# Kernel tuning notes

Measured on AMD Instinct MI355X. Metric: run time of the kernel, lower is better.

Reference implementation:

```python
import jax, jax.numpy as jnp
import numpy as np

DIM = 768
HEADS = 12
HD = DIM // HEADS
B, NX, NY = 8, 1024, 1024
GRID = 32
FREQ = 100.0
MLP_HID = 4 * DIM
EPS = 1e-5


def _grid_pos(batch, n, grid):
    g = int(np.sqrt(n))
    yy, xx = jnp.meshgrid(jnp.arange(g, dtype=jnp.int32), jnp.arange(g, dtype=jnp.int32), indexing='ij')
    pos = jnp.stack([yy.reshape(-1), xx.reshape(-1)], axis=-1)  # [N,2]
    return jnp.broadcast_to(pos[None], (batch, n, 2))


def setup_inputs() -> dict:
    key = jax.random.key(0)
    ks = jax.random.split(key, 16)
    s = 0.02
    inp = {
        'x': jax.random.normal(ks[0], (B, NX, DIM), jnp.float32),
        'y': jax.random.normal(ks[1], (B, NY, DIM), jnp.float32),
        'xpos': _grid_pos(B, NX, GRID),
        'ypos': _grid_pos(B, NY, GRID),
        # norms (gamma, beta)
        'norm1_g': jnp.ones((DIM,), jnp.float32), 'norm1_b': jnp.zeros((DIM,), jnp.float32),
        'norm2_g': jnp.ones((DIM,), jnp.float32), 'norm2_b': jnp.zeros((DIM,), jnp.float32),
        'norm3_g': jnp.ones((DIM,), jnp.float32), 'norm3_b': jnp.zeros((DIM,), jnp.float32),
        'normy_g': jnp.ones((DIM,), jnp.float32), 'normy_b': jnp.zeros((DIM,), jnp.float32),
        # self-attn: fused qkv (no bias, qkv_bias=False), out proj (with bias)
        'qkv_w': jax.random.normal(ks[2], (DIM, 3 * DIM), jnp.float32) * s,
        'attn_proj_w': jax.random.normal(ks[3], (DIM, DIM), jnp.float32) * s,
        'attn_proj_b': jnp.zeros((DIM,), jnp.float32),
        # cross-attn: separate q/k/v (no bias), out proj (with bias)
        'projq_w': jax.random.normal(ks[4], (DIM, DIM), jnp.float32) * s,
        'projk_w': jax.random.normal(ks[5], (DIM, DIM), jnp.float32) * s,
        'projv_w': jax.random.normal(ks[6], (DIM, DIM), jnp.float32) * s,
        'cross_proj_w': jax.random.normal(ks[7], (DIM, DIM), jnp.float32) * s,
        'cross_proj_b': jnp.zeros((DIM,), jnp.float32),
        # MLP
        'fc1_w': jax.random.normal(ks[8], (DIM, MLP_HID), jnp.float32) * s,
        'fc1_b': jnp.zeros((MLP_HID,), jnp.float32),
        'fc2_w': jax.random.normal(ks[9], (MLP_HID, DIM), jnp.float32) * s,
        'fc2_b': jnp.zeros((DIM,), jnp.float32),
    }
    return inp


def layernorm(x, g, b):
    m = jnp.mean(x, axis=-1, keepdims=True)
    v = jnp.mean(jnp.square(x - m), axis=-1, keepdims=True)
    return (x - m) * jax.lax.rsqrt(v + EPS) * g + b


def rope1d(tok, pos):
    # tok: [B,H,N,D], pos: [B,N] int
    D = tok.shape[-1]
    inv = 1.0 / (FREQ ** (jnp.arange(0, D, 2, dtype=jnp.float32) / D))  # [D/2]
    f = pos[:, None, :, None].astype(jnp.float32) * inv  # [B,1,N,D/2]
    emb = jnp.concatenate([f, f], axis=-1)  # [B,1,N,D]
    cos, sin = jnp.cos(emb), jnp.sin(emb)
    t1, t2 = jnp.split(tok, 2, axis=-1)
    rot = jnp.concatenate([-t2, t1], axis=-1)
    return tok * cos + rot * sin


def rope2d(tok, pos):
    # first half of head dim rotated by y-coord, second half by x-coord
    ty, tx = jnp.split(tok, 2, axis=-1)
    return jnp.concatenate([rope1d(ty, pos[..., 0]), rope1d(tx, pos[..., 1])], axis=-1)


def sdpa(q, k, v):
    scale = q.shape[-1] ** -0.5
    a = jax.nn.softmax(jnp.einsum('bhqd,bhkd->bhqk', q, k) * scale, axis=-1)
    return jnp.einsum('bhqk,bhkd->bhqd', a, v)


def split_heads(t):  # [B,N,C] -> [B,H,N,HD]
    Bv, N, C = t.shape
    return t.reshape(Bv, N, HEADS, HD).transpose(0, 2, 1, 3)


def merge_heads(t):  # [B,H,N,HD] -> [B,N,C]
    Bv, H, N, D = t.shape
    return t.transpose(0, 2, 1, 3).reshape(Bv, N, H * D)


def reference(x, y, xpos, ypos,
              norm1_g, norm1_b, norm2_g, norm2_b, norm3_g, norm3_b, normy_g, normy_b,
              qkv_w, attn_proj_w, attn_proj_b,
              projq_w, projk_w, projv_w, cross_proj_w, cross_proj_b,
              fc1_w, fc1_b, fc2_w, fc2_b):
    # --- self attention ---
    h = layernorm(x, norm1_g, norm1_b)
    qkv = h @ qkv_w  # [B,N,3C]
    q, k, v = (split_heads(t) for t in jnp.split(qkv, 3, axis=-1))
    q = rope2d(q, xpos)
    k = rope2d(k, xpos)
    x = x + merge_heads(sdpa(q, k, v)) @ attn_proj_w + attn_proj_b

    # --- cross attention ---
    y_ = layernorm(y, normy_g, normy_b)
    hq = layernorm(x, norm2_g, norm2_b)
    q = rope2d(split_heads(hq @ projq_w), xpos)
    k = rope2d(split_heads(y_ @ projk_w), ypos)
    v = split_heads(y_ @ projv_w)
    x = x + merge_heads(sdpa(q, k, v)) @ cross_proj_w + cross_proj_b

    # --- MLP ---
    h = layernorm(x, norm3_g, norm3_b)
    x = x + jax.nn.gelu(h @ fc1_w + fc1_b, approximate=False) @ fc2_w + fc2_b
    return (x, y)
```

## Files before the change

### kernel.cpp

```cpp
#include <hip/hip_runtime.h>
#include <hip/hip_bf16.h>
#include <math.h>

#define DIM 768
#define HEADS 12
#define HD 64
#define BB 8
#define NN 1024
#define EPSV 1e-5f

typedef unsigned int uint32;
typedef unsigned short ushort_t;
using short8 = __attribute__((ext_vector_type(8))) short;
using f32x4 = __attribute__((ext_vector_type(4))) float;

static __device__ inline ushort_t f2b(float v) {
    uint32 u = __float_as_uint(v);
    return (ushort_t)((u + 0x7FFFu + ((u >> 16) & 1u)) >> 16);
}
static __device__ inline float b2f(ushort_t v) {
    return __uint_as_float((uint32)v << 16);
}

static __device__ inline float gelu_fast(float v) {
    float v2 = v * v;
    float t1 = fmaf(0.07135481283f, v2, 1.5957691216f);
    float e = __expf(-v * t1);
    return v * __frcp_rn(1.0f + e);
}

static __device__ __forceinline__ void gload_lds16(const ushort_t* g, ushort_t* l) {
    __builtin_amdgcn_global_load_lds(
        (const __attribute__((address_space(1))) void*)g,
        (__attribute__((address_space(3))) void*)l, 16, 0, 0);
}

template <int INBF16>
__global__ __launch_bounds__(256) void ln_bf16(const void* __restrict__ in,
                                               const float* __restrict__ g,
                                               const float* __restrict__ b,
                                               ushort_t* __restrict__ out) {
    int r = blockIdx.x;
    int t = threadIdx.x;
    float v0, v1, v2;
    if (INBF16) {
        const ushort_t* x = (const ushort_t*)in + (size_t)r * DIM;
        v0 = b2f(x[t]); v1 = b2f(x[t + 256]); v2 = b2f(x[t + 512]);
    } else {
        const float* x = (const float*)in + (size_t)r * DIM;
        v0 = x[t]; v1 = x[t + 256]; v2 = x[t + 512];
    }
    ushort_t* o = out + (size_t)r * DIM;
    float s = v0 + v1 + v2;
    float s2 = v0 * v0 + v1 * v1 + v2 * v2;
    for (int off = 32; off; off >>= 1) {
        s += __shfl_xor(s, off);
        s2 += __shfl_xor(s2, off);
    }
    __shared__ float ls[4], lq[4];
    int wid = t >> 6;
    if ((t & 63) == 0) { ls[wid] = s; lq[wid] = s2; }
    __syncthreads();
    s = ls[0] + ls[1] + ls[2] + ls[3];
    s2 = lq[0] + lq[1] + lq[2] + lq[3];
    float mean = s * (1.0f / DIM);
    float var = s2 * (1.0f / DIM) - mean * mean;
    float rs = rsqrtf(var + EPSV);
    o[t]       = f2b((v0 - mean) * rs * g[t]       + b[t]);
    o[t + 256] = f2b((v1 - mean) * rs * g[t + 256] + b[t + 256]);
    o[t + 512] = f2b((v2 - mean) * rs * g[t + 512] + b[t + 512]);
}

struct XArgs {
    const float* src[8];
    ushort_t* dst[8];
    int K[8], N[8];
    int tstart[9];
};
__global__ __launch_bounds__(256) void xform_w(XArgs a) {
    __shared__ float tl[32][33];
    int t = blockIdx.x;
    int w = 0;
    while (t >= a.tstart[w + 1]) w++;
    int lt = t - a.tstart[w];
    int ntn = a.N[w] >> 5;
    int k0 = (lt / ntn) * 32, n0 = (lt % ntn) * 32;
    const float* src = a.src[w];
    ushort_t* dst = a.dst[w];
    int K = a.K[w], N = a.N[w];
    int rr = threadIdx.x >> 5, cc = threadIdx.x & 31;
#pragma unroll
    for (int u = 0; u < 4; u++)
        tl[rr + u * 8][cc] = src[(size_t)(k0 + rr + u * 8) * N + n0 + cc];
    __syncthreads();
#pragma unroll
    for (int u = 0; u < 4; u++)
        dst[(size_t)(n0 + rr + u * 8) * K + k0 + cc] = f2b(tl[cc][rr + u * 8]);
}

template <int ACT, int OBF16, int RESBF16>
__global__ __launch_bounds__(256) void gemm_mfma(const ushort_t* __restrict__ A,
                                                 const ushort_t* __restrict__ Wt,
                                                 const float* __restrict__ bias,
                                                 const void* res,
                                                 void* Cout, int M, int N, int K) {
    __shared__ ushort_t lds[4][128 * 32];
    int bid = blockIdx.x;
    int xcd = bid & 7, rr = bid >> 3;
    int bx = rr >> 3;
    int by = xcd * 8 + (rr & 7);
    int m0 = by * 128, n0 = bx * 128;
    int tid = threadIdx.x;
    int wid = tid >> 6, lane = tid & 63;
    int wm = wid >> 1, wn = wid & 1;
    int l15 = lane & 15, lh = lane >> 4;

    int srow = lane >> 2, cslot = lane & 3;

    auto STAGE = [&](int buf, int k0) {
#pragma unroll
        for (int inst = 0; inst < 2; inst++) {
            int r0 = (wid * 2 + inst) * 16 + srow;
            int swzr = (r0 & 3) ^ ((r0 >> 2) & 3);
            int csrc = (cslot ^ swzr) << 3;
            gload_lds16(A + (size_t)(m0 + r0) * K + k0 + csrc,
                        &lds[buf * 2 + 0][(wid * 2 + inst) * 512]);
            gload_lds16(Wt + (size_t)(n0 + r0) * K + k0 + csrc,
                        &lds[buf * 2 + 1][(wid * 2 + inst) * 512]);
        }
    };

    STAGE(0, 0);
    f32x4 acc[4][4] = {};
    __syncthreads();

    int nT = K >> 5;
    int cur = 0;
    for (int t = 0; t < nT; t++) {
        if (t + 1 < nT) STAGE(cur ^ 1, (t + 1) << 5);
        short8 af[4], bfr[4];
#pragma unroll
        for (int i = 0; i < 4; i++) {
            int rA = wm * 64 + i * 16 + l15;
            int sA = lh ^ ((rA & 3) ^ ((rA >> 2) & 3));
            af[i] = *(const short8*)&lds[cur * 2 + 0][rA * 32 + (sA << 3)];
            int rB = wn * 64 + i * 16 + l15;
            int sB = lh ^ ((rB & 3) ^ ((rB >> 2) & 3));
            bfr[i] = *(const short8*)&lds[cur * 2 + 1][rB * 32 + (sB << 3)];
        }
#pragma unroll
        for (int i = 0; i < 4; i++)
#pragma unroll
            for (int j = 0; j < 4; j++)
                acc[i][j] = __builtin_amdgcn_mfma_f32_16x16x32_bf16(
                    af[i], bfr[j], acc[i][j], 0, 0, 0);
        __syncthreads();
        cur ^= 1;
    }

    float* ep = (float*)&lds[0][0] + wid * 1088;
    int erow = lane >> 2, ecol = (lane & 3) * 16;
#pragma unroll
    for (int i = 0; i < 4; i++) {
#pragma unroll
        for (int j = 0; j < 4; j++) {
            int n = n0 + wn * 64 + j * 16 + l15;
            float bv = bias ? bias[n] : 0.0f;
#pragma unroll
            for (int r = 0; r < 4; r++) {
                float v = acc[i][j][r] + bv;
                if (ACT == 1) v = gelu_fast(v);
                ep[(lh * 4 + r) * 68 + j * 16 + l15] = v;
            }
        }
        int m = m0 + wm * 64 + i * 16 + erow;
        size_t off = (size_t)m * N + n0 + wn * 64 + ecol;
        float vv[16];
#pragma unroll
        for (int u = 0; u < 4; u++)
            *(float4*)&vv[u * 4] = *(float4*)&ep[erow * 68 + ecol + u * 4];
        if (res) {
            if (RESBF16) {
                uint4 rb0 = *(const uint4*)((const ushort_t*)res + off);
                uint4 rb1 = *(const uint4*)((const ushort_t*)res + off + 8);
                const ushort_t* rp0 = (const ushort_t*)&rb0;
                const ushort_t* rp1 = (const ushort_t*)&rb1;
#pragma unroll
                for (int u = 0; u < 8; u++) {
                    vv[u] += b2f(rp0[u]);
                    vv[u + 8] += b2f(rp1[u]);
                }
            } else {
#pragma unroll
                for (int u = 0; u < 4; u++) {
                    float4 rv = *(const float4*)((const float*)res + off + u * 4);
                    vv[u * 4 + 0] += rv.x;
                    vv[u * 4 + 1] += rv.y;
                    vv[u * 4 + 2] += rv.z;
                    vv[u * 4 + 3] += rv.w;
                }
            }
        }
        if (OBF16) {
            ushort_t tb[16];
#pragma unroll
            for (int u = 0; u < 16; u++) tb[u] = f2b(vv[u]);
            *(uint4*)((ushort_t*)Cout + off)     = *(uint4*)&tb[0];
            *(uint4*)((ushort_t*)Cout + off + 8) = *(uint4*)&tb[8];
        } else {
#pragma unroll
            for (int u = 0; u < 4; u++)
                *(float4*)((float*)Cout + off + u * 4) = *(float4*)&vv[u * 4];
        }
    }
}

__global__ __launch_bounds__(256) void rope2_bf16(ushort_t* __restrict__ ta,
                                                  const int* __restrict__ pa, int sa,
                                                  ushort_t* __restrict__ tb,
                                                  const int* __restrict__ pb, int sb,
                                                  int rt) {
    int idx = blockIdx.x * 256 + threadIdx.x;
    ushort_t* t;
    const int* pos;
    int rowStride;
    if (idx >= rt) { idx -= rt; t = tb; pos = pb; rowStride = sb; }
    else           { t = ta; pos = pa; rowStride = sa; }
    int i = idx & 15;
    int half = (idx >> 4) & 1;
    int h = (idx >> 5) % HEADS;
    int bn = idx / (HEADS * 32);
    int p = pos[(size_t)bn * 2 + half];
    float inv = powf(100.0f, -(float)i / 16.0f);
    float f = (float)p * inv;
    float c, s;
    sincosf(f, &s, &c);
    ushort_t* base = t + (size_t)bn * rowStride + h * HD + half * 32;
    float t1 = b2f(base[i]), t2 = b2f(base[i + 16]);
    base[i]      = f2b(t1 * c - t2 * s);
    base[i + 16] = f2b(t2 * c + t1 * s);
}

__global__ __launch_bounds__(256) void transpose_v(const ushort_t* __restrict__ src,
                                                   int ss, ushort_t* __restrict__ dst) {
    __shared__ ushort_t tl[64][66];
    int bid = blockIdx.x;
    int nt = bid & 15;
    int h = (bid >> 4) % HEADS;
    int b = bid / (16 * HEADS);
    int n0 = nt * 64;
    int t = threadIdx.x;
    int r = t >> 2, c0 = (t & 3) * 16;
    const ushort_t* s = src + ((size_t)(b * NN) + n0 + r) * ss + h * HD + c0;
    *(uint4*)&tl[r][c0]     = *(const uint4*)s;
    *(uint4*)&tl[r][c0 + 8] = *(const uint4*)(s + 8);
    __syncthreads();
    ushort_t* d = dst + (((size_t)(b * HEADS + h)) * HD + r) * NN + n0 + c0;
    ushort_t tmp[16];
#pragma unroll
    for (int u = 0; u < 16; u++) tmp[u] = tl[c0 + u][r];
    *(uint4*)d       = *(uint4*)tmp;
    *(uint4*)(d + 8) = *(uint4*)(tmp + 8);
}

__global__ __launch_bounds__(256) void attn_mfma(const ushort_t* __restrict__ Q, int sq,
                                                 const ushort_t* __restrict__ K, int sk,
                                                 const ushort_t* __restrict__ VT,
                                                 ushort_t* __restrict__ O, int so) {
    __shared__ ushort_t Qs[64][72];
    __shared__ ushort_t Kb[2][64 * 64];
    __shared__ ushort_t Vb[2][64 * 64];
    __shared__ ushort_t Ps[64][72];

    int g = blockIdx.x;
    int bid = (g & 7) * 192 + (g >> 3);
    int qb = bid & 15;
    int h = (bid >> 4) % HEADS;
    int b = bid / (16 * HEADS);
    int n0 = qb * 64;

    int tid = threadIdx.x;
    int lane = tid & 63, wq = tid >> 6;
    int l15 = lane & 15, lh = lane >> 4;
    int xr = l15 & 7;

    const ushort_t* Qbase = Q + (size_t)b * NN * sq + h * HD;
    const ushort_t* Kbase = K + (size_t)b * NN * sk + h * HD;
    const ushort_t* VTbase = VT + ((size_t)(b * HEADS + h)) * HD * NN;
    ushort_t* Obase = O + (size_t)b * NN * so + h * HD;

    int row = tid >> 2, ch = (tid & 3) * 2;
    int c0 = ch << 3;
    int wo0 = row * 64 + ((ch ^ (row & 7)) << 3);
    int wo1 = row * 64 + (((ch + 1) ^ (row & 7)) << 3);

    {
        const ushort_t* src = Qbase + (size_t)(n0 + row) * sq + c0;
        uint4 q0 = *(const uint4*)src;
        uint4 q1 = *(const uint4*)(src + 8);
        ushort_t* qp0 = (ushort_t*)&q0;
        ushort_t* qp1 = (ushort_t*)&q1;
        ushort_t t0[8], t1[8];
#pragma unroll
        for (int u = 0; u < 8; u++) {
            t0[u] = f2b(b2f(qp0[u]) * 0.125f);
            t1[u] = f2b(b2f(qp1[u]) * 0.125f);
        }
        *(uint4*)&Qs[row][c0]     = *(uint4*)t0;
        *(uint4*)&Qs[row][c0 + 8] = *(uint4*)t1;
    }

    const ushort_t* kp = Kbase + (size_t)row * sk + c0;
    const ushort_t* vp = VTbase + (size_t)row * NN + c0;

    uint4 rk0 = *(const uint4*)kp, rk1 = *(const uint4*)(kp + 8);
    uint4 rv0 = *(const uint4*)vp, rv1 = *(const uint4*)(vp + 8);
    *(uint4*)&Kb[0][wo0] = rk0;
    *(uint4*)&Kb[0][wo1] = rk1;
    *(uint4*)&Vb[0][wo0] = rv0;
    *(uint4*)&Vb[0][wo1] = rv1;
    {
        const ushort_t* kp2 = kp + (size_t)64 * sk;
        const ushort_t* vp2 = vp + 64;
        rk0 = *(const uint4*)kp2;
        rk1 = *(const uint4*)(kp2 + 8);
        rv0 = *(const uint4*)vp2;
        rv1 = *(const uint4*)(vp2 + 8);
    }

    short8 ones;
#pragma unroll
    for (int u = 0; u < 8; u++) ones[u] = (short)0x3F80;

    f32x4 oacc[4] = {};
    f32x4 oaccS = {};

    __syncthreads();

    for (int kt = 0; kt < NN / 64; kt++) {
        int cb = kt & 1;
        if (kt + 1 < NN / 64) {
            *(uint4*)&Kb[cb ^ 1][wo0] = rk0;
            *(uint4*)&Kb[cb ^ 1][wo1] = rk1;
            *(uint4*)&Vb[cb ^ 1][wo0] = rv0;
            *(uint4*)&Vb[cb ^ 1][wo1] = rv1;
        }
        if (kt + 2 < NN / 64) {
            const ushort_t* kp2 = kp + (size_t)(kt + 2) * 64 * sk;
            const ushort_t* vp2 = vp + (size_t)(kt + 2) * 64;
            rk0 = *(const uint4*)kp2;
            rk1 = *(const uint4*)(kp2 + 8);
            rv0 = *(const uint4*)vp2;
            rv1 = *(const uint4*)(vp2 + 8);
        }

        f32x4 s[4] = {};
#pragma unroll
        for (int ks8 = 0; ks8 < 2; ks8++) {
            short8 aq = *(const short8*)&Qs[wq * 16 + l15][ks8 * 32 + lh * 8];
#pragma unroll
            for (int j = 0; j < 4; j++) {
                int cc = (ks8 * 4 + lh) ^ xr;
                short8 bk = *(const short8*)&Kb[cb][(j * 16 + l15) * 64 + (cc << 3)];
                s[j] = __builtin_amdgcn_mfma_f32_16x16x32_bf16(aq, bk, s[j], 0, 0, 0);
            }
        }

#pragma unroll
        for (int r = 0; r < 4; r++) {
            float p0 = __expf(s[0][r]), p1 = __expf(s[1][r]);
            float p2 = __expf(s[2][r]), p3 = __expf(s[3][r]);
            int qrow = wq * 16 + lh * 4 + r;
            Ps[qrow][0 * 16 + l15] = f2b(p0);
            Ps[qrow][1 * 16 + l15] = f2b(p1);
            Ps[qrow][2 * 16 + l15] = f2b(p2);
            Ps[qrow][3 * 16 + l15] = f2b(p3);
        }

#pragma unroll
        for (int ks8 = 0; ks8 < 2; ks8++) {
            short8 ap = *(const short8*)&Ps[wq * 16 + l15][ks8 * 32 + lh * 8];
#pragma unroll
            for (int j = 0; j < 4; j++) {
                int cc = (ks8 * 4 + lh) ^ xr;
                short8 bv = *(const short8*)&Vb[cb][(j * 16 + l15) * 64 + (cc << 3)];
                oacc[j] = __builtin_amdgcn_mfma_f32_16x16x32_bf16(ap, bv, oacc[j], 0, 0, 0);
            }
            oaccS = __builtin_amdgcn_mfma_f32_16x16x32_bf16(ap, ones, oaccS, 0, 0, 0);
        }
        __syncthreads();
    }

#pragma unroll
    for (int r = 0; r < 4; r++) {
        float inv = 1.0f / oaccS[r];
        int prow = wq * 16 + lh * 4 + r;
#pragma unroll
        for (int j = 0; j < 4; j++)
            Ps[prow][j * 16 + l15] = f2b(oacc[j][r] * inv);
    }
    int erow = lane >> 2, ecol = (lane & 3) * 16;
    uint4 w0 = *(uint4*)&Ps[wq * 16 + erow][ecol];
    uint4 w1 = *(uint4*)&Ps[wq * 16 + erow][ecol + 8];
    ushort_t* op = Obase + (size_t)(n0 + wq * 16 + erow) * so + ecol;
    *(uint4*)op       = w0;
    *(uint4*)(op + 8) = w1;
}

__global__ __launch_bounds__(256) void fill_f32(float* __restrict__ out, float v, int n) {
    int i = blockIdx.x * 256 + threadIdx.x;
    if (i < n) out[i] = v;
}

extern "C" void kernel_launch(void* const* d_in, const int* in_sizes, int n_in,
                              void* d_out, int out_size, void* d_ws, size_t ws_size,
                              hipStream_t stream) {
    const float* x = (const float*)d_in[0];
    const float* y = (const float*)d_in[1];
    const int* xpos = (const int*)d_in[2];
    const int* ypos = (const int*)d_in[3];
    const float* norm1_g = (const float*)d_in[4];
    const float* norm1_b = (const float*)d_in[5];
    const float* norm2_g = (const float*)d_in[6];
    const float* norm2_b = (const float*)d_in[7];
    const float* norm3_g = (const float*)d_in[8];
    const float* norm3_b = (const float*)d_in[9];
    const float* normy_g = (const float*)d_in[10];
    const float* normy_b = (const float*)d_in[11];
    const float* qkv_w = (const float*)d_in[12];
    const float* attn_proj_w = (const float*)d_in[13];
    const float* attn_proj_b = (const float*)d_in[14];
    const float* projq_w = (const float*)d_in[15];
    const float* projk_w = (const float*)d_in[16];
    const float* projv_w = (const float*)d_in[17];
    const float* cross_proj_w = (const float*)d_in[18];
    const float* cross_proj_b = (const float*)d_in[19];
    const float* fc1_w = (const float*)d_in[20];
    const float* fc1_b = (const float*)d_in[21];
    const float* fc2_w = (const float*)d_in[22];
    const float* fc2_b = (const float*)d_in[23];
    float* out = (float*)d_out;

    const size_t SZ = (size_t)BB * NN * DIM;
    const int ROWS = BB * NN;

    const size_t WS_NEED = SZ * 4 + SZ * 2 + 4 * SZ * 2 + 9437184ull * 2;

    {
        const int expect[24] = {
            (int)SZ, (int)SZ, BB * NN * 2, BB * NN * 2,
            DIM, DIM, DIM, DIM, DIM, DIM, DIM, DIM,
            DIM * 3 * DIM, DIM * DIM, DIM,
            DIM * DIM, DIM * DIM, DIM * DIM, DIM * DIM, DIM,
            DIM * 4 * DIM, 4 * DIM, 4 * DIM * DIM, DIM};
        float sentinel = 0.0f;
        if (n_in != 24) sentinel = 2000.0f;
        else {
            for (int i = 0; i < 24; i++)
                if (in_sizes[i] != expect[i]) { sentinel = 1000.0f + i; break; }
        }
        if (sentinel == 0.0f && ws_size < WS_NEED) sentinel = 3000.0f;
        if (sentinel == 0.0f && out_size != (int)(2 * SZ)) sentinel = 4000.0f;
        if (sentinel != 0.0f) {
            fill_f32<<<(int)((SZ + 255) / 256), 256, 0, stream>>>(out, sentinel, (int)SZ);
            return;
        }
    }

    ushort_t* bufXb = (ushort_t*)d_ws;
    ushort_t* bufAb = (ushort_t*)((float*)d_ws + SZ);
    ushort_t* bufQKVb = bufAb + SZ;
    ushort_t* wts = bufQKVb + 4 * SZ;

    ushort_t* qkvT = wts;
    ushort_t* apT  = qkvT + 2304 * 768;
    ushort_t* pqT  = apT + 768 * 768;
    ushort_t* pkT  = pqT + 768 * 768;
    ushort_t* pvT  = pkT + 768 * 768;
    ushort_t* cpT  = pvT + 768 * 768;
    ushort_t* fc1T = cpT + 768 * 768;
    ushort_t* fc2T = fc1T + 3072 * 768;
    ushort_t* HID  = bufQKVb;

    XArgs xa;
    xa.src[0] = qkv_w;        xa.dst[0] = qkvT; xa.K[0] = 768;  xa.N[0] = 2304;
    xa.src[1] = attn_proj_w;  xa.dst[1] = apT;  xa.K[1] = 768;  xa.N[1] = 768;
    xa.src[2] = projq_w;      xa.dst[2] = pqT;  xa.K[2] = 768;  xa.N[2] = 768;
    xa.src[3] = projk_w;      xa.dst[3] = pkT;  xa.K[3] = 768;  xa.N[3] = 768;
    xa.src[4] = projv_w;      xa.dst[4] = pvT;  xa.K[4] = 768;  xa.N[4] = 768;
    xa.src[5] = cross_proj_w; xa.dst[5] = cpT;  xa.K[5] = 768;  xa.N[5] = 768;
    xa.src[6] = fc1_w;        xa.dst[6] = fc1T; xa.K[6] = 768;  xa.N[6] = 3072;
    xa.src[7] = fc2_w;        xa.dst[7] = fc2T; xa.K[7] = 3072; xa.N[7] = 768;
    int acc_t = 0;
    for (int i = 0; i < 8; i++) {
        xa.tstart[i] = acc_t;
        acc_t += (xa.K[i] / 32) * (xa.N[i] / 32);
    }
    xa.tstart[8] = acc_t;
    xform_w<<<acc_t, 256, 0, stream>>>(xa);

    const int rt = ROWS * HEADS * 32;
    const int attnGrid = BB * HEADS * (NN / 64);
    ushort_t* VTg;

    ln_bf16<0><<<ROWS, 256, 0, stream>>>(x, norm1_g, norm1_b, bufAb);
    gemm_mfma<0, 1, 0><<<64 * 18, 256, 0, stream>>>(bufAb, qkvT, nullptr, nullptr,
                                                    bufQKVb, ROWS, 2304, 768);
    rope2_bf16<<<2 * rt / 256, 256, 0, stream>>>(bufQKVb, xpos, 2304,
                                                 bufQKVb + DIM, xpos, 2304, rt);
    VTg = bufQKVb + 3 * SZ;
    transpose_v<<<attnGrid, 256, 0, stream>>>(bufQKVb + 2 * DIM, 2304, VTg);
    attn_mfma<<<attnGrid, 256, 0, stream>>>(bufQKVb, 2304, bufQKVb + DIM, 2304,
                                            VTg, bufAb, DIM);
    gemm_mfma<0, 1, 0><<<64 * 6, 256, 0, stream>>>(bufAb, apT, attn_proj_b, x,
                                                   bufXb, ROWS, 768, 768);

    ushort_t* Qc = bufQKVb;
    ushort_t* KVc = bufQKVb + SZ;
    ln_bf16<1><<<ROWS, 256, 0, stream>>>(bufXb, norm2_g, norm2_b, bufAb);
    gemm_mfma<0, 1, 0><<<64 * 6, 256, 0, stream>>>(bufAb, pqT, nullptr, nullptr,
                                                   Qc, ROWS, 768, 768);
    ln_bf16<0><<<ROWS, 256, 0, stream>>>(y, normy_g, normy_b, bufAb);
    gemm_mfma<0, 1, 0><<<64 * 12, 256, 0, stream>>>(bufAb, pkT, nullptr, nullptr,
                                                    KVc, ROWS, 1536, 768);
    rope2_bf16<<<2 * rt / 256, 256, 0, stream>>>(Qc, xpos, 768,
                                                 KVc, ypos, 1536, rt);
    VTg = bufQKVb + 3 * SZ;
    transpose_v<<<attnGrid, 256, 0, stream>>>(KVc + DIM, 1536, VTg);
    attn_mfma<<<attnGrid, 256, 0, stream>>>(Qc, 768, KVc, 1536, VTg, bufAb, DIM);
    gemm_mfma<0, 1, 1><<<64 * 6, 256, 0, stream>>>(bufAb, cpT, cross_proj_b, bufXb,
                                                   bufXb, ROWS, 768, 768);

    ln_bf16<1><<<ROWS, 256, 0, stream>>>(bufXb, norm3_g, norm3_b, bufAb);
    gemm_mfma<1, 1, 0><<<64 * 24, 256, 0, stream>>>(bufAb, fc1T, fc1_b, nullptr,
                                                    HID, ROWS, 3072, 768);
    gemm_mfma<0, 0, 1><<<64 * 6, 256, 0, stream>>>(HID, fc2T, fc2_b, bufXb,
                                                   out, ROWS, 768, 3072);

    hipMemcpyAsync(out + SZ, y, SZ * sizeof(float), hipMemcpyDeviceToDevice, stream);
}
```

Baseline: 478.2 us.

## Enlarge GEMM block tile to 256x128 with each wave owning 64x128

The MFMA GEMM block tile grows from 128x128 to 256x128. Each of the four waves now computes a 64-row by 128-column strip with 4x8 accumulators, and all waves share the full B tile from LDS. The LDS staging, epilogue and grid launch sizes are adjusted to match, and bias values are hoisted out of the epilogue loop. The aim is more reuse of each staged B tile and fewer global loads per FLOP. The cost is higher register and LDS use, and half as many blocks, so the N=768 GEMMs launch only 192 blocks, which may leave CUs idle.

```diff
diff --git a/kernel.cpp b/kernel.cpp
--- a/kernel.cpp
+++ b/kernel.cpp
@@ -104,95 +104,106 @@
                                                  const float* __restrict__ bias,
                                                  const void* res,
                                                  void* Cout, int M, int N, int K) {
-    __shared__ ushort_t lds[4][128 * 32];
+    __shared__ ushort_t lds[24576];
     int bid = blockIdx.x;
+    int nblk = N >> 7;
     int xcd = bid & 7, rr = bid >> 3;
-    int bx = rr >> 3;
-    int by = xcd * 8 + (rr & 7);
-    int m0 = by * 128, n0 = bx * 128;
+    int bx = rr >> 2;
+    int by = xcd * 4 + (rr & 3);
+    int m0 = by * 256, n0 = bx * 128;
     int tid = threadIdx.x;
     int wid = tid >> 6, lane = tid & 63;
-    int wm = wid >> 1, wn = wid & 1;
     int l15 = lane & 15, lh = lane >> 4;
 
-    int srow = lane >> 2, cslot = lane & 3;
-
     auto STAGE = [&](int buf, int k0) {
+        ushort_t* Ab = &lds[buf * 12288];
+        ushort_t* Bb = &lds[buf * 12288 + 8192];
+#pragma unroll
+        for (int inst = 0; inst < 4; inst++) {
+            int cid = (wid * 4 + inst) * 64 + lane;
+            int row = cid >> 2, slot = cid & 3;
+            int csrc = (slot ^ ((row & 3) ^ ((row >> 2) & 3))) << 3;
+            gload_lds16(A + (size_t)(m0 + row) * K + k0 + csrc,
+                        &Ab[(wid * 4 + inst) * 512]);
+        }
 #pragma unroll
         for (int inst = 0; inst < 2; inst++) {
-            int r0 = (wid * 2 + inst) * 16 + srow;
-            int swzr = (r0 & 3) ^ ((r0 >> 2) & 3);
-            int csrc = (cslot ^ swzr) << 3;
-            gload_lds16(A + (size_t)(m0 + r0) * K + k0 + csrc,
-                        &lds[buf * 2 + 0][(wid * 2 + inst) * 512]);
-            gload_lds16(Wt + (size_t)(n0 + r0) * K + k0 + csrc,
-                        &lds[buf * 2 + 1][(wid * 2 + inst) * 512]);
+            int cid = (wid * 2 + inst) * 64 + lane;
+            int row = cid >> 2, slot = cid & 3;
+            int csrc = (slot ^ ((row & 3) ^ ((row >> 2) & 3))) << 3;
+            gload_lds16(Wt + (size_t)(n0 + row) * K + k0 + csrc,
+                        &Bb[(wid * 2 + inst) * 512]);
         }
     };
 
     STAGE(0, 0);
-    f32x4 acc[4][4] = {};
+    f32x4 acc[4][8] = {};
     __syncthreads();
 
     int nT = K >> 5;
     int cur = 0;
     for (int t = 0; t < nT; t++) {
         if (t + 1 < nT) STAGE(cur ^ 1, (t + 1) << 5);
-        short8 af[4], bfr[4];
+        const ushort_t* Ab = &lds[cur * 12288];
+        const ushort_t* Bb = &lds[cur * 12288 + 8192];
+        short8 af[4], bfr[8];
 #pragma unroll
         for (int i = 0; i < 4; i++) {
-            int rA = wm * 64 + i * 16 + l15;
+            int rA = wid * 64 + i * 16 + l15;
             int sA = lh ^ ((rA & 3) ^ ((rA >> 2) & 3));
-            af[i] = *(const short8*)&lds[cur * 2 + 0][rA * 32 + (sA << 3)];
-            int rB = wn * 64 + i * 16 + l15;
+            af[i] = *(const short8*)&Ab[rA * 32 + (sA << 3)];
+        }
+#pragma unroll
+        for (int j = 0; j < 8; j++) {
+            int rB = j * 16 + l15;
             int sB = lh ^ ((rB & 3) ^ ((rB >> 2) & 3));
-            bfr[i] = *(const short8*)&lds[cur * 2 + 1][rB * 32 + (sB << 3)];
+            bfr[j] = *(const short8*)&Bb[rB * 32 + (sB << 3)];
         }
 #pragma unroll
         for (int i = 0; i < 4; i++)
 #pragma unroll
-            for (int j = 0; j < 4; j++)
+            for (int j = 0; j < 8; j++)
                 acc[i][j] = __builtin_amdgcn_mfma_f32_16x16x32_bf16(
                     af[i], bfr[j], acc[i][j], 0, 0, 0);
         __syncthreads();
         cur ^= 1;
     }
 
-    float* ep = (float*)&lds[0][0] + wid * 1088;
-    int erow = lane >> 2, ecol = (lane & 3) * 16;
+    float* ep = (float*)&lds[0] + wid * 2112;
+    float bvj[8];
+#pragma unroll
+    for (int j = 0; j < 8; j++)
+        bvj[j] = bias ? bias[n0 + j * 16 + l15] : 0.0f;
+    int erow = lane >> 2, ecol = (lane & 3) * 32;
 #pragma unroll
     for (int i = 0; i < 4; i++) {
 #pragma unroll
-        for (int j = 0; j < 4; j++) {
-            int n = n0 + wn * 64 + j * 16 + l15;
-            float bv = bias ? bias[n] : 0.0f;
+        for (int j = 0; j < 8; j++) {
 #pragma unroll
             for (int r = 0; r < 4; r++) {
-                float v = acc[i][j][r] + bv;
+                float v = acc[i][j][r] + bvj[j];
                 if (ACT == 1) v = gelu_fast(v);
-                ep[(lh * 4 + r) * 68 + j * 16 + l15] = v;
+                ep[(lh * 4 + r) * 132 + j * 16 + l15] = v;
             }
         }
-        int m = m0 + wm * 64 + i * 16 + erow;
-        size_t off = (size_t)m * N + n0 + wn * 64 + ecol;
-        float vv[16];
-#pragma unroll
-        for (int u = 0; u < 4; u++)
-            *(float4*)&vv[u * 4] = *(float4*)&ep[erow * 68 + ecol + u * 4];
+        int m = m0 + wid * 64 + i * 16 + erow;
+        size_t off = (size_t)m * N + n0 + ecol;
+        float vv[32];
+#pragma unroll
+        for (int u = 0; u < 8; u++)
+            *(float4*)&vv[u * 4] = *(float4*)&ep[erow * 132 + ecol + u * 4];
         if (res) {
             if (RESBF16) {
-                uint4 rb0 = *(const uint4*)((const ushort_t*)res + off);
-                uint4 rb1 = *(const uint4*)((const ushort_t*)res + off + 8);
-                const ushort_t* rp0 = (const ushort_t*)&rb0;
-                const ushort_t* rp1 = (const ushort_t*)&rb1;
-#pragma unroll
-                for (int u = 0; u < 8; u++) {
-                    vv[u] += b2f(rp0[u]);
-                    vv[u + 8] += b2f(rp1[u]);
+#pragma unroll
+                for (int q = 0; q < 4; q++) {
+                    uint4 rb = *(const uint4*)((const ushort_t*)res + off + q * 8);
+                    const ushort_t* rp = (const ushort_t*)&rb;
+#pragma unroll
+                    for (int u = 0; u < 8; u++) vv[q * 8 + u] += b2f(rp[u]);
                 }
             } else {
 #pragma unroll
-                for (int u = 0; u < 4; u++) {
+                for (int u = 0; u < 8; u++) {
                     float4 rv = *(const float4*)((const float*)res + off + u * 4);
                     vv[u * 4 + 0] += rv.x;
                     vv[u * 4 + 1] += rv.y;
@@ -202,17 +213,19 @@
             }
         }
         if (OBF16) {
-            ushort_t tb[16];
-#pragma unroll
-            for (int u = 0; u < 16; u++) tb[u] = f2b(vv[u]);
-            *(uint4*)((ushort_t*)Cout + off)     = *(uint4*)&tb[0];
-            *(uint4*)((ushort_t*)Cout + off + 8) = *(uint4*)&tb[8];
+            ushort_t tb[32];
+#pragma unroll
+            for (int u = 0; u < 32; u++) tb[u] = f2b(vv[u]);
+#pragma unroll
+            for (int q = 0; q < 4; q++)
+                *(uint4*)((ushort_t*)Cout + off + q * 8) = *(uint4*)&tb[q * 8];
         } else {
 #pragma unroll
-            for (int u = 0; u < 4; u++)
+            for (int u = 0; u < 8; u++)
                 *(float4*)((float*)Cout + off + u * 4) = *(float4*)&vv[u * 4];
         }
     }
+    (void)nblk;
 }
 
 __global__ __launch_bounds__(256) void rope2_bf16(ushort_t* __restrict__ ta,
@@ -501,10 +514,11 @@
 
     const int rt = ROWS * HEADS * 32;
     const int attnGrid = BB * HEADS * (NN / 64);
+    const int MT = ROWS / 256;
     ushort_t* VTg;
 
     ln_bf16<0><<<ROWS, 256, 0, stream>>>(x, norm1_g, norm1_b, bufAb);
-    gemm_mfma<0, 1, 0><<<64 * 18, 256, 0, stream>>>(bufAb, qkvT, nullptr, nullptr,
+    gemm_mfma<0, 1, 0><<<MT * 18, 256, 0, stream>>>(bufAb, qkvT, nullptr, nullptr,
                                                     bufQKVb, ROWS, 2304, 768);
     rope2_bf16<<<2 * rt / 256, 256, 0, stream>>>(bufQKVb, xpos, 2304,
                                                  bufQKVb + DIM, xpos, 2304, rt);
@@ -512,29 +526,29 @@
     transpose_v<<<attnGrid, 256, 0, stream>>>(bufQKVb + 2 * DIM, 2304, VTg);
     attn_mfma<<<attnGrid, 256, 0, stream>>>(bufQKVb, 2304, bufQKVb + DIM, 2304,
                                             VTg, bufAb, DIM);
-    gemm_mfma<0, 1, 0><<<64 * 6, 256, 0, stream>>>(bufAb, apT, attn_proj_b, x,
+    gemm_mfma<0, 1, 0><<<MT * 6, 256, 0, stream>>>(bufAb, apT, attn_proj_b, x,
                                                    bufXb, ROWS, 768, 768);
 
     ushort_t* Qc = bufQKVb;
     ushort_t* KVc = bufQKVb + SZ;
     ln_bf16<1><<<ROWS, 256, 0, stream>>>(bufXb, norm2_g, norm2_b, bufAb);
-    gemm_mfma<0, 1, 0><<<64 * 6, 256, 0, stream>>>(bufAb, pqT, nullptr, nullptr,
+    gemm_mfma<0, 1, 0><<<MT * 6, 256, 0, stream>>>(bufAb, pqT, nullptr, nullptr,
                                                    Qc, ROWS, 768, 768);
     ln_bf16<0><<<ROWS, 256, 0, stream>>>(y, normy_g, normy_b, bufAb);
-    gemm_mfma<0, 1, 0><<<64 * 12, 256, 0, stream>>>(bufAb, pkT, nullptr, nullptr,
+    gemm_mfma<0, 1, 0><<<MT * 12, 256, 0, stream>>>(bufAb, pkT, nullptr, nullptr,
                                                     KVc, ROWS, 1536, 768);
     rope2_bf16<<<2 * rt / 256, 256, 0, stream>>>(Qc, xpos, 768,
                                                  KVc, ypos, 1536, rt);
     VTg = bufQKVb + 3 * SZ;
     transpose_v<<<attnGrid, 256, 0, stream>>>(KVc + DIM, 1536, VTg);
     attn_mfma<<<attnGrid, 256, 0, stream>>>(Qc, 768, KVc, 1536, VTg, bufAb, DIM);
-    gemm_mfma<0, 1, 1><<<64 * 6, 256, 0, stream>>>(bufAb, cpT, cross_proj_b, bufXb,
+    gemm_mfma<0, 1, 1><<<MT * 6, 256, 0, stream>>>(bufAb, cpT, cross_proj_b, bufXb,
                                                    bufXb, ROWS, 768, 768);
 
     ln_bf16<1><<<ROWS, 256, 0, stream>>>(bufXb, norm3_g, norm3_b, bufAb);
-    gemm_mfma<1, 1, 0><<<64 * 24, 256, 0, stream>>>(bufAb, fc1T, fc1_b, nullptr,
+    gemm_mfma<1, 1, 0><<<MT * 24, 256, 0, stream>>>(bufAb, fc1T, fc1_b, nullptr,
                                                     HID, ROWS, 3072, 768);
-    gemm_mfma<0, 0, 1><<<64 * 6, 256, 0, stream>>>(HID, fc2T, fc2_b, bufXb,
+    gemm_mfma<0, 0, 1><<<MT * 6, 256, 0, stream>>>(HID, fc2T, fc2_b, bufXb,
                                                    out, ROWS, 768, 3072);
 
     hipMemcpyAsync(out + SZ, y, SZ * sizeof(float), hipMemcpyDeviceToDevice, stream);
```

New measurement: 589.0 us. 23.2% more time.

## Widen attention blocks to 128 query rows with 8 waves sharing K/V tiles

Applied to the files above, without the earlier changes.

The attention kernel now processes 128 query rows per block using 512 threads (8 waves), so each K/V tile staged in shared memory is reused by twice as many query rows. Global K/V traffic per query is halved and the grid shrinks to half as many blocks. Each thread now loads one 16-byte chunk of K and V per tile instead of two. The cost is larger shared memory per block and fewer blocks (768), which may lower occupancy or leave CUs unevenly loaded.

```diff
diff --git a/kernel.cpp b/kernel.cpp
--- a/kernel.cpp
+++ b/kernel.cpp
@@ -263,21 +263,21 @@
     *(uint4*)(d + 8) = *(uint4*)(tmp + 8);
 }
 
-__global__ __launch_bounds__(256) void attn_mfma(const ushort_t* __restrict__ Q, int sq,
+__global__ __launch_bounds__(512) void attn_mfma(const ushort_t* __restrict__ Q, int sq,
                                                  const ushort_t* __restrict__ K, int sk,
                                                  const ushort_t* __restrict__ VT,
                                                  ushort_t* __restrict__ O, int so) {
-    __shared__ ushort_t Qs[64][72];
+    __shared__ ushort_t Qs[128][72];
     __shared__ ushort_t Kb[2][64 * 64];
     __shared__ ushort_t Vb[2][64 * 64];
-    __shared__ ushort_t Ps[64][72];
+    __shared__ ushort_t Ps[128][72];
 
     int g = blockIdx.x;
-    int bid = (g & 7) * 192 + (g >> 3);
-    int qb = bid & 15;
-    int h = (bid >> 4) % HEADS;
-    int b = bid / (16 * HEADS);
-    int n0 = qb * 64;
+    int bid = (g & 7) * 96 + (g >> 3);
+    int qb = bid & 7;
+    int h = (bid >> 3) % HEADS;
+    int b = bid / (8 * HEADS);
+    int n0 = qb * 128;
 
     int tid = threadIdx.x;
     int lane = tid & 63, wq = tid >> 6;
@@ -289,12 +289,8 @@
     const ushort_t* VTbase = VT + ((size_t)(b * HEADS + h)) * HD * NN;
     ushort_t* Obase = O + (size_t)b * NN * so + h * HD;
 
-    int row = tid >> 2, ch = (tid & 3) * 2;
-    int c0 = ch << 3;
-    int wo0 = row * 64 + ((ch ^ (row & 7)) << 3);
-    int wo1 = row * 64 + (((ch + 1) ^ (row & 7)) << 3);
-
     {
+        int row = tid >> 2, c0 = (tid & 3) * 16;
         const ushort_t* src = Qbase + (size_t)(n0 + row) * sq + c0;
         uint4 q0 = *(const uint4*)src;
         uint4 q1 = *(const uint4*)(src + 8);
@@ -310,23 +306,18 @@
         *(uint4*)&Qs[row][c0 + 8] = *(uint4*)t1;
     }
 
-    const ushort_t* kp = Kbase + (size_t)row * sk + c0;
-    const ushort_t* vp = VTbase + (size_t)row * NN + c0;
-
-    uint4 rk0 = *(const uint4*)kp, rk1 = *(const uint4*)(kp + 8);
-    uint4 rv0 = *(const uint4*)vp, rv1 = *(const uint4*)(vp + 8);
-    *(uint4*)&Kb[0][wo0] = rk0;
-    *(uint4*)&Kb[0][wo1] = rk1;
-    *(uint4*)&Vb[0][wo0] = rv0;
-    *(uint4*)&Vb[0][wo1] = rv1;
-    {
-        const ushort_t* kp2 = kp + (size_t)64 * sk;
-        const ushort_t* vp2 = vp + 64;
-        rk0 = *(const uint4*)kp2;
-        rk1 = *(const uint4*)(kp2 + 8);
-        rv0 = *(const uint4*)vp2;
-        rv1 = *(const uint4*)(vp2 + 8);
-    }
+    int krow = tid >> 3, kch = tid & 7;
+    int kc0 = kch << 3;
+    int kwo = krow * 64 + ((kch ^ (krow & 7)) << 3);
+    const ushort_t* kp = Kbase + (size_t)krow * sk + kc0;
+    const ushort_t* vp = VTbase + (size_t)krow * NN + kc0;
+
+    uint4 rk = *(const uint4*)kp;
+    uint4 rv = *(const uint4*)vp;
+    *(uint4*)&Kb[0][kwo] = rk;
+    *(uint4*)&Vb[0][kwo] = rv;
+    rk = *(const uint4*)(kp + (size_t)64 * sk);
+    rv = *(const uint4*)(vp + 64);
 
     short8 ones;
 #pragma unroll
@@ -340,18 +331,12 @@
     for (int kt = 0; kt < NN / 64; kt++) {
         int cb = kt & 1;
         if (kt + 1 < NN / 64) {
-            *(uint4*)&Kb[cb ^ 1][wo0] = rk0;
-            *(uint4*)&Kb[cb ^ 1][wo1] = rk1;
-            *(uint4*)&Vb[cb ^ 1][wo0] = rv0;
-            *(uint4*)&Vb[cb ^ 1][wo1] = rv1;
+            *(uint4*)&Kb[cb ^ 1][kwo] = rk;
+            *(uint4*)&Vb[cb ^ 1][kwo] = rv;
         }
         if (kt + 2 < NN / 64) {
-            const ushort_t* kp2 = kp + (size_t)(kt + 2) * 64 * sk;
-            const ushort_t* vp2 = vp + (size_t)(kt + 2) * 64;
-            rk0 = *(const uint4*)kp2;
-            rk1 = *(const uint4*)(kp2 + 8);
-            rv0 = *(const uint4*)vp2;
-            rv1 = *(const uint4*)(vp2 + 8);
+            rk = *(const uint4*)(kp + (size_t)(kt + 2) * 64 * sk);
+            rv = *(const uint4*)(vp + (size_t)(kt + 2) * 64);
         }
 
         f32x4 s[4] = {};
@@ -500,7 +485,8 @@
     xform_w<<<acc_t, 256, 0, stream>>>(xa);
 
     const int rt = ROWS * HEADS * 32;
-    const int attnGrid = BB * HEADS * (NN / 64);
+    const int attnGrid = BB * HEADS * (NN / 128);
+    const int tvGrid = BB * HEADS * (NN / 64);
     ushort_t* VTg;
 
     ln_bf16<0><<<ROWS, 256, 0, stream>>>(x, norm1_g, norm1_b, bufAb);
@@ -509,8 +495,8 @@
     rope2_bf16<<<2 * rt / 256, 256, 0, stream>>>(bufQKVb, xpos, 2304,
                                                  bufQKVb + DIM, xpos, 2304, rt);
     VTg = bufQKVb + 3 * SZ;
-    transpose_v<<<attnGrid, 256, 0, stream>>>(bufQKVb + 2 * DIM, 2304, VTg);
-    attn_mfma<<<attnGrid, 256, 0, stream>>>(bufQKVb, 2304, bufQKVb + DIM, 2304,
+    transpose_v<<<tvGrid, 256, 0, stream>>>(bufQKVb + 2 * DIM, 2304, VTg);
+    attn_mfma<<<attnGrid, 512, 0, stream>>>(bufQKVb, 2304, bufQKVb + DIM, 2304,
                                             VTg, bufAb, DIM);
     gemm_mfma<0, 1, 0><<<64 * 6, 256, 0, stream>>>(bufAb, apT, attn_proj_b, x,
                                                    bufXb, ROWS, 768, 768);
@@ -526,8 +512,8 @@
     rope2_bf16<<<2 * rt / 256, 256, 0, stream>>>(Qc, xpos, 768,
                                                  KVc, ypos, 1536, rt);
     VTg = bufQKVb + 3 * SZ;
-    transpose_v<<<attnGrid, 256, 0, stream>>>(KVc + DIM, 1536, VTg);
-    attn_mfma<<<attnGrid, 256, 0, stream>>>(Qc, 768, KVc, 1536, VTg, bufAb, DIM);
+    transpose_v<<<tvGrid, 256, 0, stream>>>(KVc + DIM, 1536, VTg);
+    attn_mfma<<<attnGrid, 512, 0, stream>>>(Qc, 768, KVc, 1536, VTg, bufAb, DIM);
     gemm_mfma<0, 1, 1><<<64 * 6, 256, 0, stream>>>(bufAb, cpT, cross_proj_b, bufXb,
                                                    bufXb, ROWS, 768, 768);
 
```

New measurement: 463.2 us. 3.1% less time.
